# Optimization experiments

Hardware: AMD Instinct MI355X
Metric: run time of the kernel (lower is better)

The kernel has to match this reference:

```python
import jax, jax.numpy as jnp
import numpy as np


def setup_inputs() -> dict:
    key = jax.random.key(0)
    k1, k2, k3 = jax.random.split(key, 3)
    B, N, T_BG, T_IN = 32, 64, 512, 256
    surv_steps = jax.random.uniform(k1, (B, N, T_BG), dtype=jnp.float32)
    time_bg = jax.random.uniform(k2, (T_BG,), dtype=jnp.float32)
    time_in = jax.random.uniform(k3, (T_IN,), dtype=jnp.float32)
    bandwidth = jnp.ones((1,), dtype=jnp.float32)  # learned parameter
    return {
        "surv_steps": surv_steps,
        "time_bg": time_bg,
        "time_in": time_in,
        "bandwidth": bandwidth,
        "single_time": 0,
    }


def reference(surv_steps, time_bg, time_in, bandwidth, single_time):
    # bandwidth.clamp_min(1e-6)
    b = jnp.maximum(bandwidth, 1e-6)  # [1]
    # pairwise abs time difference: [T_in, T_bg]
    t_metric = jnp.abs(time_bg[None, :] - time_in[:, None])
    # softmin(x) == softmax(-x), over the background-time axis
    t_weights = jax.nn.softmax(-(b * t_metric), axis=-1)  # [T_in, T_bg]
    if single_time:
        # t_weights -> [T_in, 1, T_bg], surv_hist = surv_steps broadcast over middle dim
        proba = jnp.sum(t_weights[:, None, :] * surv_steps, axis=-1)
    else:
        # t_weights -> [1,1,T_in,T_bg], surv_hist = surv_steps[..., None, :]
        # sum over T_bg == contraction: [B,N,T_bg] x [T_in,T_bg] -> [B,N,T_in]
        proba = jnp.einsum("bnt,it->bni", surv_steps, t_weights)
    return proba
```

## Files before the change

### kernel.cpp

```cpp
#include <hip/hip_runtime.h>
#include <math.h>

constexpr int TBG = 512;
constexpr int TIN = 256;
constexpr int M   = 2048;

__global__ __launch_bounds__(256) void weights_kernel(
    const float* __restrict__ time_bg,
    const float* __restrict__ time_in,
    const float* __restrict__ bandwidth,
    float* __restrict__ w)
{
    const int i   = blockIdx.x;
    const int tid = threadIdx.x;
    const float b  = fmaxf(bandwidth[0], 1e-6f);
    const float ti = time_in[i];

    const float x0 = -b * fabsf(time_bg[tid]       - ti);
    const float x1 = -b * fabsf(time_bg[tid + 256] - ti);

    __shared__ float sred[8];
    const int wave = tid >> 6;
    const int lane = tid & 63;

    float m = fmaxf(x0, x1);
    #pragma unroll
    for (int off = 32; off > 0; off >>= 1)
        m = fmaxf(m, __shfl_down(m, off, 64));
    if (lane == 0) sred[wave] = m;
    __syncthreads();
    if (tid == 0)
        sred[4] = fmaxf(fmaxf(sred[0], sred[1]), fmaxf(sred[2], sred[3]));
    __syncthreads();
    const float mx = sred[4];

    const float e0 = __expf(x0 - mx);
    const float e1 = __expf(x1 - mx);

    float s = e0 + e1;
    #pragma unroll
    for (int off = 32; off > 0; off >>= 1)
        s += __shfl_down(s, off, 64);
    __syncthreads();
    if (lane == 0) sred[wave] = s;
    __syncthreads();
    if (tid == 0)
        sred[5] = 1.0f / (sred[0] + sred[1] + sred[2] + sred[3]);
    __syncthreads();
    const float inv = sred[5];

    w[i * TBG + tid]       = e0 * inv;
    w[i * TBG + tid + 256] = e1 * inv;
}

constexpr int BM = 64, BN = 32, BK = 32;
constexpr int LDK = BK + 4;

__global__ __launch_bounds__(256) void gemm_kernel(
    const float* __restrict__ A,
    const float* __restrict__ W,
    float* __restrict__ C)
{
    __shared__ float As[BM][LDK];
    __shared__ float Ws[BN][LDK];

    const int tid = threadIdx.x;
    const int tx  = tid & 15;
    const int ty  = tid >> 4;
    const int i0  = blockIdx.x * BN;
    const int m0  = blockIdx.y * BM;

    float acc[4][2] = {};

    const int ar = tid >> 2;
    const int ac = (tid & 3) << 3;
    const int wr = tid >> 3;
    const int wc = (tid & 7) << 2;

    for (int k0 = 0; k0 < TBG; k0 += BK) {
        const float4 a4a = *(const float4*)(A + (m0 + ar) * TBG + k0 + ac);
        const float4 a4b = *(const float4*)(A + (m0 + ar) * TBG + k0 + ac + 4);
        const float4 w4  = *(const float4*)(W + (i0 + wr) * TBG + k0 + wc);
        *(float4*)&As[ar][ac]     = a4a;
        *(float4*)&As[ar][ac + 4] = a4b;
        *(float4*)&Ws[wr][wc]     = w4;
        __syncthreads();

        #pragma unroll
        for (int k4 = 0; k4 < BK / 4; ++k4) {
            float4 av[4], wv[2];
            #pragma unroll
            for (int r = 0; r < 4; ++r)
                av[r] = *(const float4*)&As[ty + 16 * r][k4 * 4];
            #pragma unroll
            for (int c = 0; c < 2; ++c)
                wv[c] = *(const float4*)&Ws[tx + 16 * c][k4 * 4];
            #pragma unroll
            for (int r = 0; r < 4; ++r)
                #pragma unroll
                for (int c = 0; c < 2; ++c)
                    acc[r][c] += av[r].x * wv[c].x + av[r].y * wv[c].y
                               + av[r].z * wv[c].z + av[r].w * wv[c].w;
        }
        __syncthreads();
    }

    #pragma unroll
    for (int r = 0; r < 4; ++r)
        #pragma unroll
        for (int c = 0; c < 2; ++c)
            C[(m0 + ty + 16 * r) * TIN + i0 + tx + 16 * c] = acc[r][c];
}

extern "C" void kernel_launch(void* const* d_in, const int* in_sizes, int n_in,
                              void* d_out, int out_size, void* d_ws, size_t ws_size,
                              hipStream_t stream)
{
    const float* surv      = (const float*)d_in[0];
    const float* time_bg   = (const float*)d_in[1];
    const float* time_in   = (const float*)d_in[2];
    const float* bandwidth = (const float*)d_in[3];

    float* w = (float*)d_ws;
    float* out = (float*)d_out;

    weights_kernel<<<dim3(TIN), dim3(256), 0, stream>>>(time_bg, time_in, bandwidth, w);
    gemm_kernel<<<dim3(TIN / BN, M / BM), dim3(256), 0, stream>>>(surv, w, out);
}
```

Measured before the change: 85.19 us.

## Fuse softmin weight generation into split-K GEMM with atomic accumulation

Removes the separate weights kernel and its global weight matrix. Each GEMM block now recomputes its column normalisers and generates the exp weights on the fly into shared memory. K is split four ways, results are combined with atomic adds into an output zeroed by a memset, and the column tile is widened to 64. The softmax max subtraction is dropped, so very large bandwidths could underflow the sums. The change also adds redundant exp work per block plus atomic and memset traffic.

```diff
diff --git a/kernel.cpp b/kernel.cpp
--- a/kernel.cpp
+++ b/kernel.cpp
@@ -5,111 +5,104 @@
 constexpr int TIN = 256;
 constexpr int M   = 2048;
 
-__global__ __launch_bounds__(256) void weights_kernel(
+constexpr int BM = 64, BN = 64, BK = 32;
+constexpr int KSPLIT = 4;
+constexpr int KC  = TBG / KSPLIT;
+constexpr int LDK = BK + 4;
+
+__global__ __launch_bounds__(256, 2) void fused_kernel(
+    const float* __restrict__ A,
     const float* __restrict__ time_bg,
     const float* __restrict__ time_in,
     const float* __restrict__ bandwidth,
-    float* __restrict__ w)
-{
-    const int i   = blockIdx.x;
-    const int tid = threadIdx.x;
-    const float b  = fmaxf(bandwidth[0], 1e-6f);
-    const float ti = time_in[i];
-
-    const float x0 = -b * fabsf(time_bg[tid]       - ti);
-    const float x1 = -b * fabsf(time_bg[tid + 256] - ti);
-
-    __shared__ float sred[8];
-    const int wave = tid >> 6;
-    const int lane = tid & 63;
-
-    float m = fmaxf(x0, x1);
-    #pragma unroll
-    for (int off = 32; off > 0; off >>= 1)
-        m = fmaxf(m, __shfl_down(m, off, 64));
-    if (lane == 0) sred[wave] = m;
-    __syncthreads();
-    if (tid == 0)
-        sred[4] = fmaxf(fmaxf(sred[0], sred[1]), fmaxf(sred[2], sred[3]));
-    __syncthreads();
-    const float mx = sred[4];
-
-    const float e0 = __expf(x0 - mx);
-    const float e1 = __expf(x1 - mx);
-
-    float s = e0 + e1;
-    #pragma unroll
-    for (int off = 32; off > 0; off >>= 1)
-        s += __shfl_down(s, off, 64);
-    __syncthreads();
-    if (lane == 0) sred[wave] = s;
-    __syncthreads();
-    if (tid == 0)
-        sred[5] = 1.0f / (sred[0] + sred[1] + sred[2] + sred[3]);
-    __syncthreads();
-    const float inv = sred[5];
-
-    w[i * TBG + tid]       = e0 * inv;
-    w[i * TBG + tid + 256] = e1 * inv;
-}
-
-constexpr int BM = 64, BN = 32, BK = 32;
-constexpr int LDK = BK + 4;
-
-__global__ __launch_bounds__(256) void gemm_kernel(
-    const float* __restrict__ A,
-    const float* __restrict__ W,
     float* __restrict__ C)
 {
+    __shared__ float tbg_s[TBG];
     __shared__ float As[BM][LDK];
-    __shared__ float Ws[BN][LDK];
+    __shared__ float Es[BN][LDK];
+    __shared__ float red[BN][4];
+    __shared__ float invS[BN];
 
     const int tid = threadIdx.x;
-    const int tx  = tid & 15;
-    const int ty  = tid >> 4;
     const int i0  = blockIdx.x * BN;
     const int m0  = blockIdx.y * BM;
+    const int kk0 = blockIdx.z * KC;
 
-    float acc[4][2] = {};
+    const float b = fmaxf(bandwidth[0], 1e-6f);
 
-    const int ar = tid >> 2;
-    const int ac = (tid & 3) << 3;
-    const int wr = tid >> 3;
-    const int wc = (tid & 7) << 2;
+    tbg_s[tid]       = time_bg[tid];
+    tbg_s[tid + 256] = time_bg[tid + 256];
+    __syncthreads();
 
-    for (int k0 = 0; k0 < TBG; k0 += BK) {
-        const float4 a4a = *(const float4*)(A + (m0 + ar) * TBG + k0 + ac);
-        const float4 a4b = *(const float4*)(A + (m0 + ar) * TBG + k0 + ac + 4);
-        const float4 w4  = *(const float4*)(W + (i0 + wr) * TBG + k0 + wc);
+    {
+        const int   i  = tid >> 2;
+        const int   q  = tid & 3;
+        const float ti = time_in[i0 + i];
+        float s = 0.f;
+        #pragma unroll 4
+        for (int j = 0; j < 128; ++j)
+            s += __expf(-b * fabsf(tbg_s[q * 128 + j] - ti));
+        red[i][q] = s;
+    }
+    __syncthreads();
+    if (tid < BN)
+        invS[tid] = 1.0f / (red[tid][0] + red[tid][1] + red[tid][2] + red[tid][3]);
+
+    const int   ar   = tid >> 2;
+    const int   ac   = (tid & 3) << 3;
+    const float ti_e = time_in[i0 + ar];
+
+    const int tx = tid & 15;
+    const int ty = tid >> 4;
+
+    float acc[4][4] = {};
+
+    for (int k0 = 0; k0 < KC; k0 += BK) {
+        const int kk = kk0 + k0;
+
+        const float4 a4a = *(const float4*)(A + (m0 + ar) * TBG + kk + ac);
+        const float4 a4b = *(const float4*)(A + (m0 + ar) * TBG + kk + ac + 4);
+
+        float e[8];
+        #pragma unroll
+        for (int j = 0; j < 8; ++j)
+            e[j] = __expf(-b * fabsf(tbg_s[kk + ac + j] - ti_e));
+
         *(float4*)&As[ar][ac]     = a4a;
         *(float4*)&As[ar][ac + 4] = a4b;
-        *(float4*)&Ws[wr][wc]     = w4;
+        *(float4*)&Es[ar][ac]     = make_float4(e[0], e[1], e[2], e[3]);
+        *(float4*)&Es[ar][ac + 4] = make_float4(e[4], e[5], e[6], e[7]);
         __syncthreads();
 
         #pragma unroll
         for (int k4 = 0; k4 < BK / 4; ++k4) {
-            float4 av[4], wv[2];
+            float4 av[4], ev[4];
             #pragma unroll
             for (int r = 0; r < 4; ++r)
                 av[r] = *(const float4*)&As[ty + 16 * r][k4 * 4];
             #pragma unroll
-            for (int c = 0; c < 2; ++c)
-                wv[c] = *(const float4*)&Ws[tx + 16 * c][k4 * 4];
+            for (int c = 0; c < 4; ++c)
+                ev[c] = *(const float4*)&Es[tx + 16 * c][k4 * 4];
             #pragma unroll
             for (int r = 0; r < 4; ++r)
                 #pragma unroll
-                for (int c = 0; c < 2; ++c)
-                    acc[r][c] += av[r].x * wv[c].x + av[r].y * wv[c].y
-                               + av[r].z * wv[c].z + av[r].w * wv[c].w;
+                for (int c = 0; c < 4; ++c)
+                    acc[r][c] += av[r].x * ev[c].x + av[r].y * ev[c].y
+                               + av[r].z * ev[c].z + av[r].w * ev[c].w;
         }
         __syncthreads();
     }
 
+    float is[4];
+    #pragma unroll
+    for (int c = 0; c < 4; ++c)
+        is[c] = invS[tx + 16 * c];
     #pragma unroll
     for (int r = 0; r < 4; ++r)
         #pragma unroll
-        for (int c = 0; c < 2; ++c)
-            C[(m0 + ty + 16 * r) * TIN + i0 + tx + 16 * c] = acc[r][c];
+        for (int c = 0; c < 4; ++c)
+            unsafeAtomicAdd(&C[(m0 + ty + 16 * r) * TIN + i0 + tx + 16 * c],
+                            acc[r][c] * is[c]);
 }
 
 extern "C" void kernel_launch(void* const* d_in, const int* in_sizes, int n_in,
@@ -121,9 +114,10 @@
     const float* time_in   = (const float*)d_in[2];
     const float* bandwidth = (const float*)d_in[3];
 
-    float* w = (float*)d_ws;
     float* out = (float*)d_out;
 
-    weights_kernel<<<dim3(TIN), dim3(256), 0, stream>>>(time_bg, time_in, bandwidth, w);
-    gemm_kernel<<<dim3(TIN / BN, M / BM), dim3(256), 0, stream>>>(surv, w, out);
+    hipMemsetAsync(out, 0, (size_t)out_size * sizeof(float), stream);
+
+    fused_kernel<<<dim3(TIN / BN, M / BM, KSPLIT), dim3(256), 0, stream>>>(
+        surv, time_bg, time_in, bandwidth, out);
 }
```

Result: faster. 81.53 us (-4.3%).
